# Kernel tuning notes

Measured on AMD Instinct MI355X. Metric: run time of the kernel, lower is better.

The kernel has to match this reference:

```python
import jax, jax.numpy as jnp
import numpy as np

N = 50000      # nodes
E = 600000     # edges
D = 128        # embedding_dim
H = 256        # GENConv MLP hidden = 2*D (expansion=2, num_layers=2)
L = 2          # n_layers
EPS_MSG = 1e-7
EPS_NORM = 1e-5


def setup_inputs() -> dict:
    key = jax.random.key(0)
    ks = jax.random.split(key, 16)
    s = 0.05
    inp = {}
    inp["x"] = jax.random.normal(ks[0], (N, 1), jnp.float32)
    inp["edge_index"] = jax.random.randint(ks[1], (2, E), 0, N)
    inp["edge_attr"] = jax.random.normal(ks[2], (E, 1), jnp.float32)
    # encoders
    inp["Wn"] = jax.random.normal(ks[3], (1, D), jnp.float32) * s
    inp["bn_b"] = jnp.zeros((D,), jnp.float32)
    inp["We"] = jax.random.normal(ks[4], (1, D), jnp.float32) * s
    inp["be"] = jnp.zeros((D,), jnp.float32)
    # per-layer BatchNorm affine
    inp["bn_gamma"] = jnp.ones((L, D), jnp.float32)
    inp["bn_beta"] = jnp.zeros((L, D), jnp.float32)
    # per-layer GENConv params: learnable temperature t, MLP [D->H->D] with LayerNorm
    inp["t"] = jnp.ones((L,), jnp.float32)
    inp["W1"] = jax.random.normal(ks[5], (L, D, H), jnp.float32) * s
    inp["b1"] = jnp.zeros((L, H), jnp.float32)
    inp["ln_g"] = jnp.ones((L, H), jnp.float32)
    inp["ln_b"] = jnp.zeros((L, H), jnp.float32)
    inp["W2"] = jax.random.normal(ks[6], (L, H, D), jnp.float32) * s
    inp["b2"] = jnp.zeros((L, D), jnp.float32)
    return inp


def _segment_softmax(logits, seg, num):
    # per-channel softmax over edges grouped by destination node
    m = jax.ops.segment_max(logits, seg, num_segments=num)
    m = jnp.where(jnp.isfinite(m), m, 0.0)  # empty segments
    ex = jnp.exp(logits - m[seg])
    den = jax.ops.segment_sum(ex, seg, num_segments=num)
    return ex / (den[seg] + 1e-16)


def reference(x, edge_index, edge_attr, Wn, bn_b, We, be,
              bn_gamma, bn_beta, t, W1, b1, ln_g, ln_b, W2, b2):
    src, dst = edge_index[0], edge_index[1]
    h = x @ Wn + bn_b                 # [N, D] node encoder
    e = edge_attr @ We + be           # [E, D] edge encoder
    for l in range(L):
        # DeepGCNLayer 'res+': h_in -> BN -> ReLU -> conv -> + h_in
        mu = h.mean(axis=0)
        var = h.var(axis=0)
        hn = (h - mu) / jnp.sqrt(var + EPS_NORM) * bn_gamma[l] + bn_beta[l]
        hn = jax.nn.relu(hn)
        # GENConv: msg = relu(x_j + e) + eps; softmax-aggr with temperature t
        msg = jax.nn.relu(hn[src] + e) + EPS_MSG          # [E, D]
        alpha = _segment_softmax(msg * t[l], dst, N)      # [E, D]
        agg = jax.ops.segment_sum(msg * alpha, dst, num_segments=N)  # [N, D]
        out = agg + hn                                    # add root
        # GENConv MLP: Linear -> LayerNorm -> ReLU -> Linear
        z = out @ W1[l] + b1[l]
        zm = z.mean(axis=-1, keepdims=True)
        zv = z.var(axis=-1, keepdims=True)
        z = (z - zm) / jnp.sqrt(zv + EPS_NORM) * ln_g[l] + ln_b[l]
        z = jax.nn.relu(z)
        z = z @ W2[l] + b2[l]
        h = h + z                                         # res+ residual
    # DotProductPredictor over the same edge list
    return (h[src] * h[dst]).sum(axis=-1)                 # [E]
```

## Files before the change

kernel.cpp:

```cpp
#include <hip/hip_runtime.h>
#include <hip/hip_bf16.h>
#include <math.h>

#define NN 50000
#define NE 600000
#define MPAD 50048
#define NT (MPAD / 32)
#define DIM 128
#define HID 256
#define NB 49
#define HIST_BLOCKS ((NE + 255) / 256)
#define CAST_BLOCKS ((4 * DIM * HID) / 256)
#define EPS_MSG 1e-7f
#define EPS_NORM 1e-5f

typedef __attribute__((ext_vector_type(8))) short short8v;
typedef __attribute__((ext_vector_type(8))) unsigned short ushort8v;
typedef __attribute__((ext_vector_type(4))) float f32x4;

__device__ inline ushort f2bf(float f) {
    union { float f; unsigned u; } v; v.f = f;
    unsigned r = v.u + 0x7FFF + ((v.u >> 16) & 1);
    return (ushort)(r >> 16);
}
__device__ inline float bf2f(ushort u) {
    union { unsigned u; float f; } v; v.u = (unsigned)u << 16; return v.f;
}

__global__ __launch_bounds__(256) void k_setup(const float* __restrict__ x,
                                               const int* __restrict__ dst,
                                               const float* __restrict__ W1,
                                               const float* __restrict__ W2,
                                               float* __restrict__ xs,
                                               int* __restrict__ deg,
                                               ushort* __restrict__ W1t,
                                               ushort* __restrict__ W2t) {
    int b = blockIdx.x;
    if (b < 64) {
        int lane = threadIdx.x & 63;
        float s = 0.f, q = 0.f;
        for (int i = b * 256 + threadIdx.x; i < NN; i += 64 * 256) {
            float v = x[i];
            s += v; q += v * v;
        }
        #pragma unroll
        for (int off = 32; off >= 1; off >>= 1) {
            s += __shfl_xor(s, off, 64);
            q += __shfl_xor(q, off, 64);
        }
        if (lane == 0) { atomicAdd(&xs[0], s); atomicAdd(&xs[1], q); }
    } else if (b < 64 + HIST_BLOCKS) {
        int i = (b - 64) * 256 + threadIdx.x;
        if (i < NE) atomicAdd(&deg[dst[i]], 1);
    } else {
        const int chunk = DIM * HID;
        int i = (b - 64 - HIST_BLOCKS) * 256 + threadIdx.x;
        int w = i / chunk;
        int j = i - w * chunk;
        if (w < 2) {
            int r = j / HID, c = j - r * HID;
            W1t[(size_t)w * chunk + (size_t)c * DIM + r] = f2bf(W1[(size_t)w * chunk + j]);
        } else {
            int l = w - 2;
            int r = j / DIM, c = j - r * DIM;
            W2t[(size_t)l * chunk + (size_t)c * HID + r] = f2bf(W2[(size_t)l * chunk + j]);
        }
    }
}

__global__ void k_hn0(const float* __restrict__ x, const float* __restrict__ xs,
                      const float* __restrict__ Wn, const float* __restrict__ bnb,
                      const float* __restrict__ gamma, const float* __restrict__ beta,
                      ushort* __restrict__ hn, int total4) {
    int i = blockIdx.x * blockDim.x + threadIdx.x;
    if (i >= total4) return;
    int d4 = (i & 31) * 4;
    int n = i >> 5;
    float mx = xs[0] * (1.f / NN);
    float vx = xs[1] * (1.f / NN) - mx * mx;
    float xv = x[n];
    float4 w = *(const float4*)(Wn + d4);
    float4 b = *(const float4*)(bnb + d4);
    float4 g = *(const float4*)(gamma + d4);
    float4 bt = *(const float4*)(beta + d4);
    ushort4 o;
    {
        float mu = fmaf(mx, w.x, b.x), sc = rsqrtf(vx * w.x * w.x + EPS_NORM) * g.x;
        o.x = f2bf(fmaxf(fmaf(fmaf(xv, w.x, b.x) - mu, sc, bt.x), 0.f));
    }
    {
        float mu = fmaf(mx, w.y, b.y), sc = rsqrtf(vx * w.y * w.y + EPS_NORM) * g.y;
        o.y = f2bf(fmaxf(fmaf(fmaf(xv, w.y, b.y) - mu, sc, bt.y), 0.f));
    }
    {
        float mu = fmaf(mx, w.z, b.z), sc = rsqrtf(vx * w.z * w.z + EPS_NORM) * g.z;
        o.z = f2bf(fmaxf(fmaf(fmaf(xv, w.z, b.z) - mu, sc, bt.z), 0.f));
    }
    {
        float mu = fmaf(mx, w.w, b.w), sc = rsqrtf(vx * w.w * w.w + EPS_NORM) * g.w;
        o.w = f2bf(fmaxf(fmaf(fmaf(xv, w.w, b.w) - mu, sc, bt.w), 0.f));
    }
    *(ushort4*)(hn + (size_t)n * DIM + d4) = o;
}

__global__ __launch_bounds__(256) void k_scanA(const int* __restrict__ deg,
                                               int* __restrict__ partials, int n) {
    __shared__ int ws[4];
    int b = blockIdx.x;
    int t = threadIdx.x;
    int s = 0;
    #pragma unroll
    for (int i = 0; i < 4; ++i) {
        int idx = b * 1024 + t + i * 256;
        s += (idx < n) ? deg[idx] : 0;
    }
    #pragma unroll
    for (int off = 32; off >= 1; off >>= 1) s += __shfl_xor(s, off, 64);
    if ((t & 63) == 0) ws[t >> 6] = s;
    __syncthreads();
    if (t == 0) partials[b] = ws[0] + ws[1] + ws[2] + ws[3];
}

__global__ __launch_bounds__(64) void k_scanB(const int* __restrict__ partials,
                                              int* __restrict__ base,
                                              int* __restrict__ row_off) {
    int t = threadIdx.x;
    int v = (t < NB) ? partials[t] : 0;
    int x = v;
    #pragma unroll
    for (int off = 1; off < 64; off <<= 1) {
        int y = __shfl_up(x, off, 64);
        if (t >= off) x += y;
    }
    if (t < NB) base[t] = x - v;
    if (t == 0) row_off[NN] = NE;
}

__global__ __launch_bounds__(1024) void k_scanC(const int* __restrict__ deg,
                                                const int* __restrict__ base,
                                                int* __restrict__ row_off,
                                                int* __restrict__ cursor, int n) {
    __shared__ int wsum[16];
    int i = blockIdx.x * 1024 + threadIdx.x;
    int lane = threadIdx.x & 63;
    int wid = threadIdx.x >> 6;
    int v = (i < n) ? deg[i] : 0;
    int x = v;
    #pragma unroll
    for (int off = 1; off < 64; off <<= 1) {
        int y = __shfl_up(x, off, 64);
        if (lane >= off) x += y;
    }
    if (lane == 63) wsum[wid] = x;
    __syncthreads();
    if (wid == 0 && lane < 16) {
        int w = wsum[lane];
        #pragma unroll
        for (int off = 1; off < 16; off <<= 1) {
            int y = __shfl_up(w, off, 64);
            if (lane >= off) w += y;
        }
        wsum[lane] = w;
    }
    __syncthreads();
    int prev = (wid == 0) ? 0 : wsum[wid - 1];
    int excl = base[blockIdx.x] + prev + (x - v);
    if (i < n) { row_off[i] = excl; cursor[i] = excl; }
}

__global__ void k_scatter(const int* __restrict__ src, const int* __restrict__ dst,
                          const float* __restrict__ eattr, int* __restrict__ cursor,
                          int4* __restrict__ erec, int E) {
    int i = blockIdx.x * blockDim.x + threadIdx.x;
    if (i >= E) return;
    int d = dst[i];
    int pos = atomicAdd(&cursor[d], 1);
    erec[pos] = make_int4(src[i], i, __float_as_int(eattr[i]), 0);
}

__global__ void k_bn_relu(const float* __restrict__ h, const float* __restrict__ stats,
                          const float* __restrict__ gamma, const float* __restrict__ beta,
                          ushort* __restrict__ hn, int total4) {
    int i = blockIdx.x * blockDim.x + threadIdx.x;
    if (i >= total4) return;
    int d4 = (i & 31) * 4;
    int n = i >> 5;
    float4 v = *(const float4*)(h + (size_t)n * DIM + d4);
    float4 s = *(const float4*)(stats + d4);
    float4 q = *(const float4*)(stats + DIM + d4);
    float4 g = *(const float4*)(gamma + d4);
    float4 bt = *(const float4*)(beta + d4);
    ushort4 o;
    {
        float mu = s.x * (1.f / NN), var = q.x * (1.f / NN) - mu * mu;
        float sc = rsqrtf(var + EPS_NORM) * g.x;
        o.x = f2bf(fmaxf(fmaf(v.x - mu, sc, bt.x), 0.f));
    }
    {
        float mu = s.y * (1.f / NN), var = q.y * (1.f / NN) - mu * mu;
        float sc = rsqrtf(var + EPS_NORM) * g.y;
        o.y = f2bf(fmaxf(fmaf(v.y - mu, sc, bt.y), 0.f));
    }
    {
        float mu = s.z * (1.f / NN), var = q.z * (1.f / NN) - mu * mu;
        float sc = rsqrtf(var + EPS_NORM) * g.z;
        o.z = f2bf(fmaxf(fmaf(v.z - mu, sc, bt.z), 0.f));
    }
    {
        float mu = s.w * (1.f / NN), var = q.w * (1.f / NN) - mu * mu;
        float sc = rsqrtf(var + EPS_NORM) * g.w;
        o.w = f2bf(fmaxf(fmaf(v.w - mu, sc, bt.w), 0.f));
    }
    *(ushort4*)(hn + (size_t)n * DIM + d4) = o;
}

__global__ __launch_bounds__(256) void k_agg(const ushort* __restrict__ hn,
                                             const int4* __restrict__ erec,
                                             const int* __restrict__ row_off,
                                             const float* __restrict__ We,
                                             const float* __restrict__ be,
                                             const float* __restrict__ t_all, int l,
                                             ushort* __restrict__ ob, int N) {
    int n = blockIdx.x * 4 + (threadIdx.x >> 6);
    if (n >= N) return;
    int lane = threadIdx.x & 63;
    int d0 = lane * 2;
    float2 we = *(const float2*)(We + d0);
    float2 bd = *(const float2*)(be + d0);
    float t = t_all[l];
    int p0 = row_off[n], p1 = row_off[n + 1];
    int deg = p1 - p0;

    int mp = p0 + lane;
    int s_l = 0; float ea_l = 0.f;
    if (mp < p1) {
        int4 r = erec[mp];
        s_l = r.x; ea_l = __int_as_float(r.z);
    }

    float den0 = 0.f, num0 = 0.f, den1 = 0.f, num1 = 0.f;
    int kmax = deg < 64 ? deg : 64;
    int k = 0;
    for (; k + 4 <= kmax; k += 4) {
        int sA = __shfl(s_l, k, 64), sB = __shfl(s_l, k + 1, 64);
        int sC = __shfl(s_l, k + 2, 64), sD = __shfl(s_l, k + 3, 64);
        float eA = __shfl(ea_l, k, 64), eB = __shfl(ea_l, k + 1, 64);
        float eC = __shfl(ea_l, k + 2, 64), eD = __shfl(ea_l, k + 3, 64);
        uint hA = *(const uint*)(hn + (size_t)sA * DIM + d0);
        uint hB = *(const uint*)(hn + (size_t)sB * DIM + d0);
        uint hC = *(const uint*)(hn + (size_t)sC * DIM + d0);
        uint hD = *(const uint*)(hn + (size_t)sD * DIM + d0);
        {
            float m0 = fmaxf(bf2f((ushort)hA) + fmaf(eA, we.x, bd.x), 0.f) + EPS_MSG;
            float m1 = fmaxf(bf2f((ushort)(hA >> 16)) + fmaf(eA, we.y, bd.y), 0.f) + EPS_MSG;
            float x0 = __expf(m0 * t), x1 = __expf(m1 * t);
            den0 += x0; num0 += m0 * x0; den1 += x1; num1 += m1 * x1;
        }
        {
            float m0 = fmaxf(bf2f((ushort)hB) + fmaf(eB, we.x, bd.x), 0.f) + EPS_MSG;
            float m1 = fmaxf(bf2f((ushort)(hB >> 16)) + fmaf(eB, we.y, bd.y), 0.f) + EPS_MSG;
            float x0 = __expf(m0 * t), x1 = __expf(m1 * t);
            den0 += x0; num0 += m0 * x0; den1 += x1; num1 += m1 * x1;
        }
        {
            float m0 = fmaxf(bf2f((ushort)hC) + fmaf(eC, we.x, bd.x), 0.f) + EPS_MSG;
            float m1 = fmaxf(bf2f((ushort)(hC >> 16)) + fmaf(eC, we.y, bd.y), 0.f) + EPS_MSG;
            float x0 = __expf(m0 * t), x1 = __expf(m1 * t);
            den0 += x0; num0 += m0 * x0; den1 += x1; num1 += m1 * x1;
        }
        {
            float m0 = fmaxf(bf2f((ushort)hD) + fmaf(eD, we.x, bd.x), 0.f) + EPS_MSG;
            float m1 = fmaxf(bf2f((ushort)(hD >> 16)) + fmaf(eD, we.y, bd.y), 0.f) + EPS_MSG;
            float x0 = __expf(m0 * t), x1 = __expf(m1 * t);
            den0 += x0; num0 += m0 * x0; den1 += x1; num1 += m1 * x1;
        }
    }
    for (; k < kmax; ++k) {
        int s = __shfl(s_l, k, 64);
        float ea = __shfl(ea_l, k, 64);
        uint hv = *(const uint*)(hn + (size_t)s * DIM + d0);
        float m0 = fmaxf(bf2f((ushort)hv) + fmaf(ea, we.x, bd.x), 0.f) + EPS_MSG;
        float m1 = fmaxf(bf2f((ushort)(hv >> 16)) + fmaf(ea, we.y, bd.y), 0.f) + EPS_MSG;
        float x0 = __expf(m0 * t), x1 = __expf(m1 * t);
        den0 += x0; num0 += m0 * x0; den1 += x1; num1 += m1 * x1;
    }
    for (int p = p0 + 64; p < p1; ++p) {
        int4 r = erec[p];
        int s = r.x;
        float ea = __int_as_float(r.z);
        uint hv = *(const uint*)(hn + (size_t)s * DIM + d0);
        float m0 = fmaxf(bf2f((ushort)hv) + fmaf(ea, we.x, bd.x), 0.f) + EPS_MSG;
        float m1 = fmaxf(bf2f((ushort)(hv >> 16)) + fmaf(ea, we.y, bd.y), 0.f) + EPS_MSG;
        float x0 = __expf(m0 * t), x1 = __expf(m1 * t);
        den0 += x0; num0 += m0 * x0; den1 += x1; num1 += m1 * x1;
    }
    uint hr = *(const uint*)(hn + (size_t)n * DIM + d0);
    float a0 = (deg > 0) ? num0 / (den0 + 1e-16f) : 0.f;
    float a1 = (deg > 0) ? num1 / (den1 + 1e-16f) : 0.f;
    uint o = (uint)f2bf(a0 + bf2f((ushort)hr)) |
             ((uint)f2bf(a1 + bf2f((ushort)(hr >> 16))) << 16);
    *(uint*)(ob + (size_t)n * DIM + d0) = o;
}

template <int FIRST>
__global__ __launch_bounds__(256, 2) void k_mlp(const ushort* __restrict__ A,
                                                const ushort* __restrict__ B1t,
                                                const float* __restrict__ b1,
                                                const float* __restrict__ g,
                                                const float* __restrict__ bv,
                                                const ushort* __restrict__ B2t,
                                                const float* __restrict__ b2,
                                                const float* __restrict__ x,
                                                const float* __restrict__ Wn,
                                                const float* __restrict__ bnb,
                                                float* __restrict__ C,
                                                ushort* __restrict__ hb,
                                                float* __restrict__ stats) {
    constexpr int LDZ = 264;
    __shared__ ushort Zs[32 * LDZ];
    __shared__ float red_s[4][32];
    __shared__ float red_q[4][32];
    __shared__ float murs[2][32];
    const int tid = threadIdx.x;
    const int lane = tid & 63;
    const int wid = tid >> 6;
    const int wc = wid * 64;
    const int wc2 = wid * 32;
    const int l15 = lane & 15;
    const int lq = lane >> 4;

    short8v bw1[4][4];
    #pragma unroll
    for (int ks = 0; ks < 4; ++ks)
        #pragma unroll
        for (int f = 0; f < 4; ++f)
            bw1[ks][f] = *(const short8v*)(B1t + (size_t)(wc + f * 16 + l15) * DIM +
                                           ks * 32 + lq * 8);
    short8v bw2[8][2];
    #pragma unroll
    for (int ks = 0; ks < 8; ++ks)
        #pragma unroll
        for (int f = 0; f < 2; ++f)
            bw2[ks][f] = *(const short8v*)(B2t + (size_t)(wc2 + f * 16 + l15) * HID +
                                           ks * 32 + lq * 8);
    float bb[4], gg[4], lb[4];
    #pragma unroll
    for (int ni = 0; ni < 4; ++ni) {
        int col = wc + ni * 16 + l15;
        bb[ni] = b1[col]; gg[ni] = g[col]; lb[ni] = bv[col];
    }
    float b2v[2], wnc[2], bnc[2];
    #pragma unroll
    for (int ni = 0; ni < 2; ++ni) {
        int col = wc2 + ni * 16 + l15;
        b2v[ni] = b2[col];
        wnc[ni] = FIRST ? Wn[col] : 0.f;
        bnc[ni] = FIRST ? bnb[col] : 0.f;
    }

    for (int tile = blockIdx.x; tile < NT; tile += gridDim.x) {
        const int row0 = tile * 32;
        short8v afr[4][2];
        #pragma unroll
        for (int ks = 0; ks < 4; ++ks)
            #pragma unroll
            for (int f = 0; f < 2; ++f)
                afr[ks][f] = *(const short8v*)(A + (size_t)(row0 + f * 16 + l15) * DIM +
                                               ks * 32 + lq * 8);
        f32x4 acc[2][4] = {};
        #pragma unroll
        for (int ks = 0; ks < 4; ++ks)
            #pragma unroll
            for (int mi = 0; mi < 2; ++mi)
                #pragma unroll
                for (int ni = 0; ni < 4; ++ni)
                    acc[mi][ni] = __builtin_amdgcn_mfma_f32_16x16x32_bf16(
                        afr[ks][mi], bw1[ks][ni], acc[mi][ni], 0, 0, 0);

        #pragma unroll
        for (int mi = 0; mi < 2; ++mi) {
            #pragma unroll
            for (int j = 0; j < 4; ++j) {
                float s = 0.f, q = 0.f;
                #pragma unroll
                for (int ni = 0; ni < 4; ++ni) {
                    float v = acc[mi][ni][j] + bb[ni];
                    acc[mi][ni][j] = v;
                    s += v; q += v * v;
                }
                #pragma unroll
                for (int off = 1; off <= 8; off <<= 1) {
                    s += __shfl_xor(s, off, 64);
                    q += __shfl_xor(q, off, 64);
                }
                if (l15 == 0) {
                    int row = mi * 16 + lq * 4 + j;
                    red_s[wid][row] = s;
                    red_q[wid][row] = q;
                }
            }
        }
        __syncthreads();
        if (tid < 32) {
            float s = red_s[0][tid] + red_s[1][tid] + red_s[2][tid] + red_s[3][tid];
            float q = red_q[0][tid] + red_q[1][tid] + red_q[2][tid] + red_q[3][tid];
            float mu = s * (1.f / HID);
            float var = q * (1.f / HID) - mu * mu;
            murs[0][tid] = mu;
            murs[1][tid] = rsqrtf(var + EPS_NORM);
        }
        __syncthreads();
        #pragma unroll
        for (int mi = 0; mi < 2; ++mi) {
            #pragma unroll
            for (int j = 0; j < 4; ++j) {
                int row = mi * 16 + lq * 4 + j;
                float mu = murs[0][row], rs = murs[1][row];
                #pragma unroll
                for (int ni = 0; ni < 4; ++ni) {
                    float v = fmaxf(fmaf((acc[mi][ni][j] - mu) * rs, gg[ni], lb[ni]), 0.f);
                    Zs[row * LDZ + wc + ni * 16 + l15] = f2bf(v);
                }
            }
        }
        __syncthreads();

        f32x4 acc2[2][2] = {};
        #pragma unroll
        for (int ks = 0; ks < 8; ++ks) {
            short8v af2[2];
            #pragma unroll
            for (int f = 0; f < 2; ++f)
                af2[f] = *(const short8v*)(Zs + (f * 16 + l15) * LDZ + ks * 32 + lq * 8);
            #pragma unroll
            for (int mi = 0; mi < 2; ++mi)
                #pragma unroll
                for (int ni = 0; ni < 2; ++ni)
                    acc2[mi][ni] = __builtin_amdgcn_mfma_f32_16x16x32_bf16(
                        af2[mi], bw2[ks][ni], acc2[mi][ni], 0, 0, 0);
        }

        float ssum[2] = {0.f, 0.f};
        float sq[2] = {0.f, 0.f};
        #pragma unroll
        for (int ni = 0; ni < 2; ++ni) {
            int col = wc2 + ni * 16 + l15;
            #pragma unroll
            for (int mi = 0; mi < 2; ++mi) {
                int rowb = row0 + mi * 16 + lq * 4;
                #pragma unroll
                for (int j = 0; j < 4; ++j) {
                    int gr = rowb + j;
                    float base;
                    if (FIRST) {
                        float xv = (gr < NN) ? x[gr] : 0.f;
                        base = fmaf(xv, wnc[ni], bnc[ni]);
                    } else {
                        base = C[(size_t)gr * DIM + col];
                    }
                    float v = acc2[mi][ni][j] + b2v[ni] + base;
                    if (FIRST) {
                        C[(size_t)gr * DIM + col] = v;
                        bool ok = gr < NN;
                        ssum[ni] += ok ? v : 0.f;
                        sq[ni] += ok ? v * v : 0.f;
                    } else {
                        hb[(size_t)gr * DIM + col] = f2bf(v);
                    }
                }
            }
        }
        if (FIRST) {
            #pragma unroll
            for (int ni = 0; ni < 2; ++ni) {
                float s = ssum[ni], q = sq[ni];
                s += __shfl_xor(s, 16, 64); s += __shfl_xor(s, 32, 64);
                q += __shfl_xor(q, 16, 64); q += __shfl_xor(q, 32, 64);
                if (lq == 0) {
                    int col = wc2 + ni * 16 + l15;
                    atomicAdd(&stats[col], s);
                    atomicAdd(&stats[DIM + col], q);
                }
            }
        }
        __syncthreads();
    }
}

__global__ __launch_bounds__(256) void k_dot(const ushort* __restrict__ hb,
                                             const int4* __restrict__ erec,
                                             const int* __restrict__ row_off,
                                             float* __restrict__ out, int N) {
    int n = blockIdx.x * 4 + (threadIdx.x >> 6);
    if (n >= N) return;
    int lane = threadIdx.x & 63;
    int sub = lane >> 4;
    int l16 = lane & 15;
    float hd[8];
    {
        ushort8v hv = *(const ushort8v*)(hb + (size_t)n * DIM + l16 * 8);
        #pragma unroll
        for (int j = 0; j < 8; ++j) hd[j] = bf2f(hv[j]);
    }
    int p0 = row_off[n], p1 = row_off[n + 1];
    int deg = p1 - p0;
    int mp = p0 + lane;
    int s_l = 0, e_l = 0;
    if (mp < p1) {
        int4 r = erec[mp];
        s_l = r.x; e_l = r.y;
    }
    int kmax = deg < 64 ? deg : 64;
    for (int k = 0; k < kmax; k += 4) {
        int idx = k + sub;
        bool ok = idx < kmax;
        int s = __shfl(s_l, idx, 64);
        int e = __shfl(e_l, idx, 64);
        ushort8v av = *(const ushort8v*)(hb + (size_t)(ok ? s : n) * DIM + l16 * 8);
        float p = 0.f;
        #pragma unroll
        for (int j = 0; j < 8; ++j) p = fmaf(bf2f(av[j]), hd[j], p);
        p += __shfl_xor(p, 1, 16);
        p += __shfl_xor(p, 2, 16);
        p += __shfl_xor(p, 4, 16);
        p += __shfl_xor(p, 8, 16);
        if (ok && l16 == 0) out[e] = p;
    }
    for (int pb = p0 + 64; pb < p1; pb += 4) {
        int pe = pb + sub;
        bool ok = pe < p1;
        int s = n, e = 0;
        if (ok) { int4 r = erec[pe]; s = r.x; e = r.y; }
        ushort8v av = *(const ushort8v*)(hb + (size_t)s * DIM + l16 * 8);
        float p = 0.f;
        #pragma unroll
        for (int j = 0; j < 8; ++j) p = fmaf(bf2f(av[j]), hd[j], p);
        p += __shfl_xor(p, 1, 16);
        p += __shfl_xor(p, 2, 16);
        p += __shfl_xor(p, 4, 16);
        p += __shfl_xor(p, 8, 16);
        if (ok && l16 == 0) out[e] = p;
    }
}

extern "C" void kernel_launch(void* const* d_in, const int* in_sizes, int n_in,
                              void* d_out, int out_size, void* d_ws, size_t ws_size,
                              hipStream_t stream) {
    const float* x        = (const float*)d_in[0];
    const int*   ei       = (const int*)d_in[1];
    const float* eattr    = (const float*)d_in[2];
    const float* Wn       = (const float*)d_in[3];
    const float* bnb      = (const float*)d_in[4];
    const float* We       = (const float*)d_in[5];
    const float* be       = (const float*)d_in[6];
    const float* bn_gamma = (const float*)d_in[7];
    const float* bn_beta  = (const float*)d_in[8];
    const float* t_all    = (const float*)d_in[9];
    const float* W1       = (const float*)d_in[10];
    const float* b1       = (const float*)d_in[11];
    const float* ln_g     = (const float*)d_in[12];
    const float* ln_b     = (const float*)d_in[13];
    const float* W2       = (const float*)d_in[14];
    const float* b2       = (const float*)d_in[15];
    float* out = (float*)d_out;

    const int N = NN, E = NE, D = DIM, H = HID;
    const int* src = ei;
    const int* dst = ei + E;

    char* ws = (char*)d_ws;
    auto alloc = [&](size_t bytes) {
        char* p = ws;
        ws += (bytes + 255) & ~(size_t)255;
        return p;
    };
    float*  h       = (float*)alloc((size_t)MPAD * D * 4);
    ushort* ob      = (ushort*)alloc((size_t)MPAD * D * 2);
    ushort* hn      = (ushort*)alloc((size_t)MPAD * D * 2);
    ushort* hb      = (ushort*)alloc((size_t)MPAD * D * 2);
    ushort* W1t     = (ushort*)alloc((size_t)2 * D * H * 2);
    ushort* W2t     = (ushort*)alloc((size_t)2 * D * H * 2);
    int4*   erec    = (int4*)alloc((size_t)E * 16);
    int*    row_off = (int*)alloc((size_t)(N + 1) * 4);
    int*    cursor  = (int*)alloc((size_t)N * 4);
    int*    deg     = (int*)alloc((size_t)N * 4);
    int*    partials= (int*)alloc((size_t)64 * 4);
    int*    pbase   = (int*)alloc((size_t)64 * 4);
    float*  stats   = (float*)alloc((size_t)2 * D * 4);
    float*  xs      = (float*)alloc((size_t)2 * 4);

    hipMemsetAsync(deg, 0, (size_t)N * 4, stream);
    hipMemsetAsync(stats, 0, 1024 + 8, stream);

    k_setup<<<64 + HIST_BLOCKS + CAST_BLOCKS, 256, 0, stream>>>(x, dst, W1, W2,
                                                                xs, deg, W1t, W2t);
    k_scanA<<<NB, 256, 0, stream>>>(deg, partials, N);
    k_scanB<<<1, 64, 0, stream>>>(partials, pbase, row_off);
    k_scanC<<<NB, 1024, 0, stream>>>(deg, pbase, row_off, cursor, N);
    k_scatter<<<(E + 255) / 256, 256, 0, stream>>>(src, dst, eattr, cursor, erec, E);
    k_hn0<<<(N * 32 + 255) / 256, 256, 0, stream>>>(x, xs, Wn, bnb, bn_gamma, bn_beta,
                                                    hn, N * 32);

    k_agg<<<(N + 3) / 4, 256, 0, stream>>>(hn, erec, row_off, We, be, t_all, 0, ob, N);
    k_mlp<1><<<512, 256, 0, stream>>>(ob, W1t, b1, ln_g, ln_b, W2t, b2,
                                      x, Wn, bnb, h, hb, stats);
    k_bn_relu<<<(N * 32 + 255) / 256, 256, 0, stream>>>(h, stats, bn_gamma + D, bn_beta + D,
                                                        hn, N * 32);

    k_agg<<<(N + 3) / 4, 256, 0, stream>>>(hn, erec, row_off, We, be, t_all, 1, ob, N);
    k_mlp<0><<<512, 256, 0, stream>>>(ob, W1t + (size_t)D * H, b1 + H,
                                      ln_g + H, ln_b + H, W2t + (size_t)D * H, b2 + D,
                                      x, Wn, bnb, h, hb, stats);

    k_dot<<<(N + 3) / 4, 256, 0, stream>>>(hb, erec, row_off, out, N);
}
```

Baseline: 361.7 us.

## Stage MLP weights in LDS, prefetch next A tile, widen aggregation unroll

The MLP kernel now keeps W1 and W2 in padded shared memory (about 133KB) instead of holding them in registers. It prefetches the next tile's A fragments and the residual/x values early so their loads overlap the MFMA work. The grid is halved to 256 blocks to match one block per CU. The aggregation gather loop is unrolled by 8 instead of 4 so more independent loads are in flight. This trades register pressure for LDS traffic and possible bank conflicts, and relies on a large LDS allocation.

```diff
diff --git a/kernel.cpp b/kernel.cpp
--- a/kernel.cpp
+++ b/kernel.cpp
@@ -241,36 +241,20 @@
     float den0 = 0.f, num0 = 0.f, den1 = 0.f, num1 = 0.f;
     int kmax = deg < 64 ? deg : 64;
     int k = 0;
-    for (; k + 4 <= kmax; k += 4) {
-        int sA = __shfl(s_l, k, 64), sB = __shfl(s_l, k + 1, 64);
-        int sC = __shfl(s_l, k + 2, 64), sD = __shfl(s_l, k + 3, 64);
-        float eA = __shfl(ea_l, k, 64), eB = __shfl(ea_l, k + 1, 64);
-        float eC = __shfl(ea_l, k + 2, 64), eD = __shfl(ea_l, k + 3, 64);
-        uint hA = *(const uint*)(hn + (size_t)sA * DIM + d0);
-        uint hB = *(const uint*)(hn + (size_t)sB * DIM + d0);
-        uint hC = *(const uint*)(hn + (size_t)sC * DIM + d0);
-        uint hD = *(const uint*)(hn + (size_t)sD * DIM + d0);
-        {
-            float m0 = fmaxf(bf2f((ushort)hA) + fmaf(eA, we.x, bd.x), 0.f) + EPS_MSG;
-            float m1 = fmaxf(bf2f((ushort)(hA >> 16)) + fmaf(eA, we.y, bd.y), 0.f) + EPS_MSG;
-            float x0 = __expf(m0 * t), x1 = __expf(m1 * t);
-            den0 += x0; num0 += m0 * x0; den1 += x1; num1 += m1 * x1;
-        }
-        {
-            float m0 = fmaxf(bf2f((ushort)hB) + fmaf(eB, we.x, bd.x), 0.f) + EPS_MSG;
-            float m1 = fmaxf(bf2f((ushort)(hB >> 16)) + fmaf(eB, we.y, bd.y), 0.f) + EPS_MSG;
-            float x0 = __expf(m0 * t), x1 = __expf(m1 * t);
-            den0 += x0; num0 += m0 * x0; den1 += x1; num1 += m1 * x1;
-        }
-        {
-            float m0 = fmaxf(bf2f((ushort)hC) + fmaf(eC, we.x, bd.x), 0.f) + EPS_MSG;
-            float m1 = fmaxf(bf2f((ushort)(hC >> 16)) + fmaf(eC, we.y, bd.y), 0.f) + EPS_MSG;
-            float x0 = __expf(m0 * t), x1 = __expf(m1 * t);
-            den0 += x0; num0 += m0 * x0; den1 += x1; num1 += m1 * x1;
-        }
-        {
-            float m0 = fmaxf(bf2f((ushort)hD) + fmaf(eD, we.x, bd.x), 0.f) + EPS_MSG;
-            float m1 = fmaxf(bf2f((ushort)(hD >> 16)) + fmaf(eD, we.y, bd.y), 0.f) + EPS_MSG;
+    for (; k + 8 <= kmax; k += 8) {
+        int ss[8]; float ee[8]; uint hv[8];
+        #pragma unroll
+        for (int u = 0; u < 8; ++u) {
+            ss[u] = __shfl(s_l, k + u, 64);
+            ee[u] = __shfl(ea_l, k + u, 64);
+        }
+        #pragma unroll
+        for (int u = 0; u < 8; ++u)
+            hv[u] = *(const uint*)(hn + (size_t)ss[u] * DIM + d0);
+        #pragma unroll
+        for (int u = 0; u < 8; ++u) {
+            float m0 = fmaxf(bf2f((ushort)hv[u]) + fmaf(ee[u], we.x, bd.x), 0.f) + EPS_MSG;
+            float m1 = fmaxf(bf2f((ushort)(hv[u] >> 16)) + fmaf(ee[u], we.y, bd.y), 0.f) + EPS_MSG;
             float x0 = __expf(m0 * t), x1 = __expf(m1 * t);
             den0 += x0; num0 += m0 * x0; den1 += x1; num1 += m1 * x1;
         }
@@ -303,20 +287,24 @@
 }
 
 template <int FIRST>
-__global__ __launch_bounds__(256, 2) void k_mlp(const ushort* __restrict__ A,
-                                                const ushort* __restrict__ B1t,
-                                                const float* __restrict__ b1,
-                                                const float* __restrict__ g,
-                                                const float* __restrict__ bv,
-                                                const ushort* __restrict__ B2t,
-                                                const float* __restrict__ b2,
-                                                const float* __restrict__ x,
-                                                const float* __restrict__ Wn,
-                                                const float* __restrict__ bnb,
-                                                float* __restrict__ C,
-                                                ushort* __restrict__ hb,
-                                                float* __restrict__ stats) {
-    constexpr int LDZ = 264;
+__global__ __launch_bounds__(256) void k_mlp(const ushort* __restrict__ A,
+                                             const ushort* __restrict__ B1t,
+                                             const float* __restrict__ b1,
+                                             const float* __restrict__ g,
+                                             const float* __restrict__ bv,
+                                             const ushort* __restrict__ B2t,
+                                             const float* __restrict__ b2,
+                                             const float* __restrict__ x,
+                                             const float* __restrict__ Wn,
+                                             const float* __restrict__ bnb,
+                                             float* __restrict__ C,
+                                             ushort* __restrict__ hb,
+                                             float* __restrict__ stats) {
+    constexpr int LW1 = 132;
+    constexpr int LW2 = 260;
+    constexpr int LDZ = 258;
+    __shared__ ushort W1s[256 * LW1];
+    __shared__ ushort W2s[128 * LW2];
     __shared__ ushort Zs[32 * LDZ];
     __shared__ float red_s[4][32];
     __shared__ float red_q[4][32];
@@ -329,20 +317,18 @@
     const int l15 = lane & 15;
     const int lq = lane >> 4;
 
-    short8v bw1[4][4];
-    #pragma unroll
-    for (int ks = 0; ks < 4; ++ks)
-        #pragma unroll
-        for (int f = 0; f < 4; ++f)
-            bw1[ks][f] = *(const short8v*)(B1t + (size_t)(wc + f * 16 + l15) * DIM +
-                                           ks * 32 + lq * 8);
-    short8v bw2[8][2];
-    #pragma unroll
-    for (int ks = 0; ks < 8; ++ks)
-        #pragma unroll
-        for (int f = 0; f < 2; ++f)
-            bw2[ks][f] = *(const short8v*)(B2t + (size_t)(wc2 + f * 16 + l15) * HID +
-                                           ks * 32 + lq * 8);
+    #pragma unroll
+    for (int i = 0; i < 16; ++i) {
+        int e = (tid + i * 256) * 8;
+        int r = e >> 7, c = e & 127;
+        *(short8v*)(W1s + r * LW1 + c) = *(const short8v*)(B1t + r * 128 + c);
+    }
+    #pragma unroll
+    for (int i = 0; i < 16; ++i) {
+        int e = (tid + i * 256) * 8;
+        int r = e >> 8, c = e & 255;
+        *(short8v*)(W2s + r * LW2 + c) = *(const short8v*)(B2t + r * 256 + c);
+    }
     float bb[4], gg[4], lb[4];
     #pragma unroll
     for (int ni = 0; ni < 4; ++ni) {
@@ -357,25 +343,68 @@
         wnc[ni] = FIRST ? Wn[col] : 0.f;
         bnc[ni] = FIRST ? bnb[col] : 0.f;
     }
-
-    for (int tile = blockIdx.x; tile < NT; tile += gridDim.x) {
+    __syncthreads();
+
+    int tile = blockIdx.x;
+    short8v afr[4][2];
+    if (tile < NT) {
+        #pragma unroll
+        for (int ks = 0; ks < 4; ++ks)
+            #pragma unroll
+            for (int f = 0; f < 2; ++f)
+                afr[ks][f] = *(const short8v*)(A + (size_t)(tile * 32 + f * 16 + l15) * DIM +
+                                               ks * 32 + lq * 8);
+    }
+
+    for (; tile < NT; tile += gridDim.x) {
         const int row0 = tile * 32;
-        short8v afr[4][2];
-        #pragma unroll
-        for (int ks = 0; ks < 4; ++ks)
-            #pragma unroll
-            for (int f = 0; f < 2; ++f)
-                afr[ks][f] = *(const short8v*)(A + (size_t)(row0 + f * 16 + l15) * DIM +
-                                               ks * 32 + lq * 8);
         f32x4 acc[2][4] = {};
         #pragma unroll
-        for (int ks = 0; ks < 4; ++ks)
+        for (int ks = 0; ks < 4; ++ks) {
+            int kk = ks * 32 + lq * 8;
+            short8v bfr[4];
+            #pragma unroll
+            for (int f = 0; f < 4; ++f)
+                bfr[f] = *(const short8v*)(W1s + (wc + f * 16 + l15) * LW1 + kk);
             #pragma unroll
             for (int mi = 0; mi < 2; ++mi)
                 #pragma unroll
                 for (int ni = 0; ni < 4; ++ni)
                     acc[mi][ni] = __builtin_amdgcn_mfma_f32_16x16x32_bf16(
-                        afr[ks][mi], bw1[ks][ni], acc[mi][ni], 0, 0, 0);
+                        afr[ks][mi], bfr[ni], acc[mi][ni], 0, 0, 0);
+        }
+
+        int nxt = tile + gridDim.x;
+        short8v afn[4][2];
+        if (nxt < NT) {
+            #pragma unroll
+            for (int ks = 0; ks < 4; ++ks)
+                #pragma unroll
+                for (int f = 0; f < 2; ++f)
+                    afn[ks][f] = *(const short8v*)(A + (size_t)(nxt * 32 + f * 16 + l15) * DIM +
+                                                   ks * 32 + lq * 8);
+        }
+        float xvv[2][4];
+        float basev[2][2][4];
+        if (FIRST) {
+            #pragma unroll
+            for (int mi = 0; mi < 2; ++mi)
+                #pragma unroll
+                for (int j = 0; j < 4; ++j) {
+                    int gr = row0 + mi * 16 + lq * 4 + j;
+                    xvv[mi][j] = (gr < NN) ? x[gr] : 0.f;
+                }
+        } else {
+            #pragma unroll
+            for (int ni = 0; ni < 2; ++ni)
+                #pragma unroll
+                for (int mi = 0; mi < 2; ++mi)
+                    #pragma unroll
+                    for (int j = 0; j < 4; ++j) {
+                        int gr = row0 + mi * 16 + lq * 4 + j;
+                        basev[ni][mi][j] = C[(size_t)gr * DIM + wc2 + ni * 16 + l15];
+                    }
+        }
 
         #pragma unroll
         for (int mi = 0; mi < 2; ++mi) {
@@ -428,16 +457,19 @@
         f32x4 acc2[2][2] = {};
         #pragma unroll
         for (int ks = 0; ks < 8; ++ks) {
-            short8v af2[2];
-            #pragma unroll
-            for (int f = 0; f < 2; ++f)
-                af2[f] = *(const short8v*)(Zs + (f * 16 + l15) * LDZ + ks * 32 + lq * 8);
+            int kk = ks * 32 + lq * 8;
+            short8v af2[2], bf2[2];
+            #pragma unroll
+            for (int f = 0; f < 2; ++f) {
+                af2[f] = *(const short8v*)(Zs + (f * 16 + l15) * LDZ + kk);
+                bf2[f] = *(const short8v*)(W2s + (wc2 + f * 16 + l15) * LW2 + kk);
+            }
             #pragma unroll
             for (int mi = 0; mi < 2; ++mi)
                 #pragma unroll
                 for (int ni = 0; ni < 2; ++ni)
                     acc2[mi][ni] = __builtin_amdgcn_mfma_f32_16x16x32_bf16(
-                        af2[mi], bw2[ks][ni], acc2[mi][ni], 0, 0, 0);
+                        af2[mi], bf2[ni], acc2[mi][ni], 0, 0, 0);
         }
 
         float ssum[2] = {0.f, 0.f};
@@ -451,13 +483,8 @@
                 #pragma unroll
                 for (int j = 0; j < 4; ++j) {
                     int gr = rowb + j;
-                    float base;
-                    if (FIRST) {
-                        float xv = (gr < NN) ? x[gr] : 0.f;
-                        base = fmaf(xv, wnc[ni], bnc[ni]);
-                    } else {
-                        base = C[(size_t)gr * DIM + col];
-                    }
+                    float base = FIRST ? fmaf(xvv[mi][j], wnc[ni], bnc[ni])
+                                       : basev[ni][mi][j];
                     float v = acc2[mi][ni][j] + b2v[ni] + base;
                     if (FIRST) {
                         C[(size_t)gr * DIM + col] = v;
@@ -482,6 +509,13 @@
                     atomicAdd(&stats[DIM + col], q);
                 }
             }
+        }
+        if (nxt < NT) {
+            #pragma unroll
+            for (int ks = 0; ks < 4; ++ks)
+                #pragma unroll
+                for (int f = 0; f < 2; ++f)
+                    afr[ks][f] = afn[ks][f];
         }
         __syncthreads();
     }
@@ -602,13 +636,13 @@
                                                     hn, N * 32);
 
     k_agg<<<(N + 3) / 4, 256, 0, stream>>>(hn, erec, row_off, We, be, t_all, 0, ob, N);
-    k_mlp<1><<<512, 256, 0, stream>>>(ob, W1t, b1, ln_g, ln_b, W2t, b2,
+    k_mlp<1><<<256, 256, 0, stream>>>(ob, W1t, b1, ln_g, ln_b, W2t, b2,
                                       x, Wn, bnb, h, hb, stats);
     k_bn_relu<<<(N * 32 + 255) / 256, 256, 0, stream>>>(h, stats, bn_gamma + D, bn_beta + D,
                                                         hn, N * 32);
 
     k_agg<<<(N + 3) / 4, 256, 0, stream>>>(hn, erec, row_off, We, be, t_all, 1, ob, N);
-    k_mlp<0><<<512, 256, 0, stream>>>(ob, W1t + (size_t)D * H, b1 + H,
+    k_mlp<0><<<256, 256, 0, stream>>>(ob, W1t + (size_t)D * H, b1 + H,
                                       ln_g + H, ln_b + H, W2t + (size_t)D * H, b2 + D,
                                       x, Wn, bnb, h, hb, stats);
 
```

Measured after the change: 366.6 us. About the same (+1.4%).
